# Performance work log

Measured on AMD Instinct MI355X. Metric: run time of the kernel, lower is better.

The kernel has to match this reference:

```python
import jax, jax.numpy as jnp
import numpy as np

B, S, H = 2, 4096, 2048
NH, NKV, D = 16, 4, 128
BS, LOCAL, GLOB, STRIDE = 64, 8, 4, 16
SEL = GLOB + LOCAL
SCALE = D ** -0.5
NEG = -1e9


def rotate_half(x):
    x1, x2 = x[..., : D // 2], x[..., D // 2 :]
    return jnp.concatenate([-x2, x1], axis=-1)


def setup_inputs():
    key = jax.random.key(0)
    ks = jax.random.split(key, 5)
    hidden_states = jax.random.normal(ks[0], (B, S, H), dtype=jnp.float32)
    # standard RoPE tables, shape [B, S, D] as the module expects (cos.unsqueeze(1))
    pos = jnp.arange(S, dtype=jnp.float32)
    inv = 1.0 / (10000.0 ** (jnp.arange(0, D, 2, dtype=jnp.float32) / D))
    freqs = pos[:, None] * inv[None, :]
    emb = jnp.concatenate([freqs, freqs], axis=-1)
    cos = jnp.broadcast_to(jnp.cos(emb)[None], (B, S, D)).astype(jnp.float32)
    sin = jnp.broadcast_to(jnp.sin(emb)[None], (B, S, D)).astype(jnp.float32)
    std = 0.02
    Wq = jax.random.normal(ks[1], (NH * D, H), dtype=jnp.float32) * std
    Wk = jax.random.normal(ks[2], (NKV * D, H), dtype=jnp.float32) * std
    Wv = jax.random.normal(ks[3], (NKV * D, H), dtype=jnp.float32) * std
    Wo = jax.random.normal(ks[4], (H, NH * D), dtype=jnp.float32) * std
    return {"hidden_states": hidden_states, "cos": cos, "sin": sin,
            "Wq": Wq, "Wk": Wk, "Wv": Wv, "Wo": Wo}


def _block_sparse_attn(q, k, v):
    # q, k, v: [B, NH, S, D]; past_len = 0, attention_mask = None (all keys valid)
    qb = S // BS
    kb = S // BS
    qid = jnp.arange(qb)
    # local blocks: the LOCAL most recent blocks ending at the query block
    loc = qid[:, None] - (LOCAL - 1 - jnp.arange(LOCAL)[None, :])
    loc = jnp.clip(loc, 0, kb - 1)
    # global blocks: strided anchors
    g = jnp.clip(jnp.arange(GLOB) * STRIDE, 0, kb - 1)
    glob = jnp.broadcast_to(g[None, :], (qb, GLOB))
    sel = jnp.concatenate([glob, loc], axis=1)  # [qb, SEL]
    valid = sel <= qid[:, None]                 # causal at block level
    # dedup: drop a selected block if an earlier slot selected the same block
    eq = sel[:, :, None] == sel[:, None, :]
    lower = jnp.tril(jnp.ones((SEL, SEL), dtype=bool), k=-1)
    keep = (~(eq & lower[None]).any(-1)) & valid  # [qb, SEL]

    k_blk = k.reshape(B, NH, kb, BS, D)
    v_blk = v.reshape(B, NH, kb, BS, D)
    k_sel = jnp.take(k_blk, sel.reshape(-1), axis=2).reshape(B, NH, qb, SEL * BS, D)
    v_sel = jnp.take(v_blk, sel.reshape(-1), axis=2).reshape(B, NH, qb, SEL * BS, D)
    q_blk = q.reshape(B, NH, qb, BS, D)

    scores = jnp.einsum("bhqid,bhqjd->bhqij", q_blk, k_sel) * SCALE  # [B,NH,qb,BS,SEL*BS]
    keep_tok = jnp.broadcast_to(keep[:, :, None], (qb, SEL, BS)).reshape(qb, SEL * BS)
    scores = scores + (1.0 - keep_tok.astype(scores.dtype))[None, None, :, None, :] * NEG
    # intra-block causal mask where selected block == query block
    same = (sel == qid[:, None]).astype(scores.dtype)  # [qb, SEL]
    intra = jnp.triu(jnp.full((BS, BS), NEG, dtype=scores.dtype), k=1)
    scores6 = scores.reshape(B, NH, qb, BS, SEL, BS)
    scores6 = scores6 + intra[None, None, None, :, None, :] * same[None, None, :, None, :, None]
    scores = scores6.reshape(B, NH, qb, BS, SEL * BS)
    probs = jax.nn.softmax(scores, axis=-1)
    out = jnp.einsum("bhqij,bhqjd->bhqid", probs, v_sel)
    return out.reshape(B, NH, S, D)


def reference(hidden_states, cos, sin, Wq, Wk, Wv, Wo):
    q = (hidden_states @ Wq.T).reshape(B, S, NH, D).transpose(0, 2, 1, 3)
    k = (hidden_states @ Wk.T).reshape(B, S, NKV, D).transpose(0, 2, 1, 3)
    v = (hidden_states @ Wv.T).reshape(B, S, NKV, D).transpose(0, 2, 1, 3)
    c = cos[:, None, :, :]
    s = sin[:, None, :, :]
    q = q * c + rotate_half(q) * s
    k = k * c + rotate_half(k) * s
    rep = NH // NKV
    k = jnp.repeat(k, rep, axis=1)
    v = jnp.repeat(v, rep, axis=1)
    out = _block_sparse_attn(q, k, v)
    out = out.transpose(0, 2, 1, 3).reshape(B, S, NH * D)
    return out @ Wo.T
```

## Files before the change

kernel.cpp:

```cpp
#include <hip/hip_runtime.h>

typedef __bf16 bf16_t;
typedef __bf16 bf16x8_t __attribute__((ext_vector_type(8)));
typedef __bf16 bf16x4_t __attribute__((ext_vector_type(4)));
typedef float f32x4_t __attribute__((ext_vector_type(4)));
typedef unsigned short u16;
typedef unsigned int u32;

#define B_ 2
#define S_ 4096
#define NH_ 16
#define NKV_ 4
#define D_ 128
#define NEG_ (-1000000000.0f)
#define SCALE_ 0.08838834764831845f

__device__ __forceinline__ void load16(const bf16_t* g, bf16_t* l) {
  __builtin_amdgcn_global_load_lds(
      (__attribute__((address_space(1))) void*)(g),
      (__attribute__((address_space(3))) void*)(l),
      16, 0, 0);
}

__global__ __launch_bounds__(256) void cvt_all_kernel(const float* __restrict__ hs,
                                                      const float* __restrict__ Wq,
                                                      const float* __restrict__ Wk,
                                                      const float* __restrict__ Wv,
                                                      const float* __restrict__ Wo,
                                                      bf16_t* __restrict__ Xb,
                                                      bf16_t* __restrict__ Wb,
                                                      bf16_t* __restrict__ Wob) {
  int i = blockIdx.x * 256 + threadIdx.x;
  const float* src; bf16_t* dst; int local;
  if (i < 4194304)      { src = hs; dst = Xb;            local = i; }
  else if (i < 5242880) { src = Wq; dst = Wb;            local = i - 4194304; }
  else if (i < 5505024) { src = Wk; dst = Wb + 4194304;  local = i - 5242880; }
  else if (i < 5767168) { src = Wv; dst = Wb + 5242880;  local = i - 5505024; }
  else                  { src = Wo; dst = Wob;           local = i - 5767168; }
  float4 v = ((const float4*)src)[local];
  bf16x4_t o;
  o.x = (bf16_t)v.x; o.y = (bf16_t)v.y; o.z = (bf16_t)v.z; o.w = (bf16_t)v.w;
  *(bf16x4_t*)(dst + (size_t)local * 4) = o;
}

template <int BF16OUT>
__global__ __launch_bounds__(256) void gemm_bt_kernel(const bf16_t* __restrict__ A,
                                                      const bf16_t* __restrict__ Bm,
                                                      float* __restrict__ Cf,
                                                      bf16_t* __restrict__ Cb,
                                                      int M, int N, int K) {
  __shared__ bf16_t As[128 * 32];
  __shared__ bf16_t Bs[128 * 32];
  const int t = threadIdx.x;
  const int lane = t & 63;
  const int w = t >> 6;
  const int wr = w >> 1, wc = w & 1;
  const int l15 = lane & 15, l4 = lane >> 4;
  const int m0 = blockIdx.x * 128;
  const int n0 = blockIdx.y * 128;
  const int xr = (l15 >> 1) & 3;

  f32x4_t acc[4][4] = {};

  for (int k0 = 0; k0 < K; k0 += 32) {
    __syncthreads();
#pragma unroll
    for (int i = 0; i < 2; i++) {
      int f = t + 256 * i;
      int row = f >> 2, cl = f & 3;
      int cg = cl ^ ((row >> 1) & 3);
      load16(A + (size_t)(m0 + row) * K + k0 + cg * 8, As + (w * 64 + i * 256) * 8);
      load16(Bm + (size_t)(n0 + row) * K + k0 + cg * 8, Bs + (w * 64 + i * 256) * 8);
    }
    __syncthreads();
    bf16x8_t af[4], bfr[4];
#pragma unroll
    for (int mi = 0; mi < 4; mi++) {
      int ra = wr * 64 + mi * 16 + l15;
      af[mi] = *(const bf16x8_t*)&As[(ra * 4 + (l4 ^ xr)) * 8];
    }
#pragma unroll
    for (int ni = 0; ni < 4; ni++) {
      int rb = wc * 64 + ni * 16 + l15;
      bfr[ni] = *(const bf16x8_t*)&Bs[(rb * 4 + (l4 ^ xr)) * 8];
    }
#pragma unroll
    for (int mi = 0; mi < 4; mi++)
#pragma unroll
      for (int ni = 0; ni < 4; ni++)
        acc[mi][ni] = __builtin_amdgcn_mfma_f32_16x16x32_bf16(af[mi], bfr[ni], acc[mi][ni], 0, 0, 0);
  }

#pragma unroll
  for (int mi = 0; mi < 4; mi++)
#pragma unroll
    for (int ni = 0; ni < 4; ni++)
#pragma unroll
      for (int r = 0; r < 4; r++) {
        int grow = m0 + wr * 64 + mi * 16 + l4 * 4 + r;
        int gcol = n0 + wc * 64 + ni * 16 + l15;
        float v = acc[mi][ni][r];
        if (BF16OUT) Cb[(size_t)grow * N + gcol] = (bf16_t)v;
        else Cf[(size_t)grow * N + gcol] = v;
      }
}

__global__ __launch_bounds__(320) void rope_kernel(const bf16_t* __restrict__ qkv,
                                                   const float* __restrict__ cosp,
                                                   const float* __restrict__ sinp,
                                                   bf16_t* __restrict__ Qro,
                                                   bf16_t* __restrict__ Kro) {
  const int tk = blockIdx.x;
  const int b = tk >> 12;
  const int s = tk & 4095;
  const int sblock = s >> 6, row = s & 63;
  const int idx = threadIdx.x;
  int head, lc;
  const bf16_t* base;
  bf16_t* outp;
  if (idx < 256) {
    head = idx >> 4; lc = idx & 15;
    base = qkv + (size_t)tk * 3072 + head * 128;
    outp = Qro + ((size_t)(b * NH_ + head) * 64 + sblock) * 8192;
  } else {
    int i2 = idx - 256;
    head = i2 >> 4; lc = i2 & 15;
    base = qkv + (size_t)tk * 3072 + 2048 + head * 128;
    outp = Kro + ((size_t)(b * NKV_ + head) * 64 + sblock) * 8192;
  }
  const int d0 = lc * 8;
  bf16x8_t x = *(const bf16x8_t*)(base + d0);
  const int d0p = (d0 < 64) ? d0 + 64 : d0 - 64;
  bf16x8_t xp = *(const bf16x8_t*)(base + d0p);
  const float sgn = (d0 < 64) ? -1.0f : 1.0f;
  const float* cb = cosp + (size_t)tk * 128 + d0;
  const float* sb = sinp + (size_t)tk * 128 + d0;
  bf16x8_t o;
#pragma unroll
  for (int e = 0; e < 8; e++)
    o[e] = (bf16_t)((float)x[e] * cb[e] + sgn * (float)xp[e] * sb[e]);
  *(bf16x8_t*)(outp + (lc * 64 + row) * 8) = o;
}

__global__ __launch_bounds__(256) void vtrans_kernel(const u16* __restrict__ qkv,
                                                     u16* __restrict__ vt) {
  __shared__ u16 tile[64][136];
  const int sblock = blockIdx.x;
  const int kh = blockIdx.y;
  const int b = blockIdx.z;
  const int t = threadIdx.x;
#pragma unroll
  for (int i = 0; i < 4; i++) {
    int f = t + 256 * i;
    int sl = f >> 4, c = f & 15;
    uint4 vv = *(const uint4*)(qkv + (size_t)(b * S_ + sblock * 64 + sl) * 3072 + 2560 + kh * 128 + c * 8);
    *(uint4*)&tile[sl][c * 8] = vv;
  }
  __syncthreads();
  u16* out = vt + ((size_t)(b * NKV_ + kh) * 64 + sblock) * 8192;
#pragma unroll
  for (int i = 0; i < 4; i++) {
    int g = t + 256 * i;
    int sc = g >> 7, d = g & 127;
    u16 e0 = tile[sc * 8 + 0][d], e1 = tile[sc * 8 + 1][d];
    u16 e2 = tile[sc * 8 + 2][d], e3 = tile[sc * 8 + 3][d];
    u16 e4 = tile[sc * 8 + 4][d], e5 = tile[sc * 8 + 5][d];
    u16 e6 = tile[sc * 8 + 6][d], e7 = tile[sc * 8 + 7][d];
    uint4 ov;
    ov.x = (u32)e0 | ((u32)e1 << 16);
    ov.y = (u32)e2 | ((u32)e3 << 16);
    ov.z = (u32)e4 | ((u32)e5 << 16);
    ov.w = (u32)e6 | ((u32)e7 << 16);
    *(uint4*)(out + (size_t)g * 8) = ov;
  }
}

__global__ __launch_bounds__(256) void attn_kernel(const bf16_t* __restrict__ Qr,
                                                   const bf16_t* __restrict__ Kr,
                                                   const bf16_t* __restrict__ Vt,
                                                   bf16_t* __restrict__ Ao) {
  __shared__ bf16_t Ks[2][8192];
  __shared__ bf16_t Vs[2][8192];
  __shared__ bf16_t Ps[4 * 16 * 72];
  const int qid = blockIdx.x;
  const int kh = blockIdx.y >> 1;
  const int hp = blockIdx.y & 1;
  const int b = blockIdx.z;
  const int t = threadIdx.x;
  const int lane = t & 63;
  const int w = t >> 6;
  const int l15 = lane & 15, l4 = lane >> 4;
  const int h = kh * 4 + hp * 2 + (w >> 1);
  int row0[2];
  row0[0] = ((w * 2) & 3) * 16;
  row0[1] = ((w * 2 + 1) & 3) * 16;

  int list[12];
  int nkeep = 0;
#pragma unroll
  for (int j = 0; j < 12; j++) {
    int cj;
    if (j < 4) cj = j * 16;
    else { cj = qid - 11 + j; cj = cj < 0 ? 0 : cj; cj = cj > 63 ? 63 : cj; }
    bool keep = (cj <= qid);
#pragma unroll
    for (int i = 0; i < j; i++) {
      int ci;
      if (i < 4) ci = i * 16;
      else { ci = qid - 11 + i; ci = ci < 0 ? 0 : ci; ci = ci > 63 ? 63 : ci; }
      if (ci == cj) keep = false;
    }
    if (keep) list[nkeep++] = cj;
  }

  const bf16_t* Qg = Qr + ((size_t)(b * NH_ + h) * 64 + qid) * 8192;
  const bf16_t* Kg = Kr + ((size_t)(b * NKV_ + kh) * 64) * 8192;
  const bf16_t* Vg = Vt + ((size_t)(b * NKV_ + kh) * 64) * 8192;

  bf16x8_t qa[2][4];
#pragma unroll
  for (int mt = 0; mt < 2; mt++)
#pragma unroll
    for (int ks = 0; ks < 4; ks++)
      qa[mt][ks] = *(const bf16x8_t*)(Qg + ((ks * 4 + l4) * 64 + row0[mt] + l15) * 8);

  bf16x8_t ones;
#pragma unroll
  for (int e = 0; e < 8; e++) ones[e] = (bf16_t)1.0f;

  float mi_r[2][4], li_r[2][4];
  f32x4_t oacc[2][8] = {};
#pragma unroll
  for (int mt = 0; mt < 2; mt++)
#pragma unroll
    for (int r = 0; r < 4; r++) { mi_r[mt][r] = -__builtin_inff(); li_r[mt][r] = 0.0f; }

  {
    int cj = list[0];
#pragma unroll
    for (int i = 0; i < 4; i++) {
      int f = t + 256 * i;
      load16(Kg + (size_t)cj * 8192 + (size_t)f * 8, Ks[0] + (w * 64 + i * 256) * 8);
      load16(Vg + (size_t)cj * 8192 + (size_t)f * 8, Vs[0] + (w * 64 + i * 256) * 8);
    }
  }

  int cur = 0;
#pragma unroll 1
  for (int idx = 0; idx < nkeep; idx++) {
    const int cj = list[idx];
    __syncthreads();
    if (idx + 1 < nkeep) {
      int cn = list[idx + 1];
#pragma unroll
      for (int i = 0; i < 4; i++) {
        int f = t + 256 * i;
        load16(Kg + (size_t)cn * 8192 + (size_t)f * 8, Ks[cur ^ 1] + (w * 64 + i * 256) * 8);
        load16(Vg + (size_t)cn * 8192 + (size_t)f * 8, Vs[cur ^ 1] + (w * 64 + i * 256) * 8);
      }
    }
    const bf16_t* ks_ = Ks[cur];
    const bf16_t* vs_ = Vs[cur];

    f32x4_t sacc[2][4] = {};
#pragma unroll
    for (int ks = 0; ks < 4; ks++)
#pragma unroll
      for (int ni = 0; ni < 4; ni++) {
        bf16x8_t kb = *(const bf16x8_t*)&ks_[((ks * 4 + l4) * 64 + ni * 16 + l15) * 8];
#pragma unroll
        for (int mt = 0; mt < 2; mt++)
          sacc[mt][ni] = __builtin_amdgcn_mfma_f32_16x16x32_bf16(qa[mt][ks], kb, sacc[mt][ni], 0, 0, 0);
      }

    const bool diag = (cj == qid);
    float alpha[2][4];
#pragma unroll
    for (int mt = 0; mt < 2; mt++) {
      float sv[4][4];
#pragma unroll
      for (int ni = 0; ni < 4; ni++)
#pragma unroll
        for (int r = 0; r < 4; r++) {
          float x = sacc[mt][ni][r] * SCALE_;
          if (diag && (ni * 16 + l15) > (row0[mt] + l4 * 4 + r)) x += NEG_;
          sv[ni][r] = x;
        }

      float rmax[4];
#pragma unroll
      for (int r = 0; r < 4; r++)
        rmax[r] = fmaxf(fmaxf(sv[0][r], sv[1][r]), fmaxf(sv[2][r], sv[3][r]));
#pragma unroll
      for (int msk = 1; msk < 16; msk <<= 1)
#pragma unroll
        for (int r = 0; r < 4; r++)
          rmax[r] = fmaxf(rmax[r], __shfl_xor(rmax[r], msk, 64));
#pragma unroll
      for (int r = 0; r < 4; r++) {
        float nm = fmaxf(mi_r[mt][r], rmax[r]);
        alpha[mt][r] = __expf(mi_r[mt][r] - nm);
        mi_r[mt][r] = nm;
      }
      float p[4][4];
#pragma unroll
      for (int ni = 0; ni < 4; ni++)
#pragma unroll
        for (int r = 0; r < 4; r++)
          p[ni][r] = __expf(sv[ni][r] - mi_r[mt][r]);
#pragma unroll
      for (int ni = 0; ni < 4; ni++)
#pragma unroll
        for (int r = 0; r < 4; r++)
          Ps[w * 1152 + (l4 * 4 + r) * 72 + ni * 16 + l15] = (bf16_t)p[ni][r];
#pragma unroll
      for (int n2 = 0; n2 < 8; n2++)
#pragma unroll
        for (int r = 0; r < 4; r++)
          oacc[mt][n2][r] *= alpha[mt][r];

      f32x4_t lacc = {};
#pragma unroll
      for (int kst = 0; kst < 2; kst++) {
        bf16x8_t pa = *(const bf16x8_t*)&Ps[w * 1152 + l15 * 72 + kst * 32 + l4 * 8];
        lacc = __builtin_amdgcn_mfma_f32_16x16x32_bf16(pa, ones, lacc, 0, 0, 0);
#pragma unroll
        for (int n2 = 0; n2 < 8; n2++) {
          bf16x8_t vb = *(const bf16x8_t*)&vs_[((kst * 4 + l4) * 128 + n2 * 16 + l15) * 8];
          oacc[mt][n2] = __builtin_amdgcn_mfma_f32_16x16x32_bf16(pa, vb, oacc[mt][n2], 0, 0, 0);
        }
      }
#pragma unroll
      for (int r = 0; r < 4; r++)
        li_r[mt][r] = li_r[mt][r] * alpha[mt][r] + lacc[r];
    }

    cur ^= 1;
  }

#pragma unroll
  for (int mt = 0; mt < 2; mt++) {
    float invl[4];
#pragma unroll
    for (int r = 0; r < 4; r++) invl[r] = 1.0f / li_r[mt][r];
#pragma unroll
    for (int n2 = 0; n2 < 8; n2++)
#pragma unroll
      for (int r = 0; r < 4; r++) {
        int m = row0[mt] + l4 * 4 + r;
        size_t idx = ((size_t)(b * S_ + qid * 64 + m)) * (NH_ * D_) + h * D_ + n2 * 16 + l15;
        Ao[idx] = (bf16_t)(oacc[mt][n2][r] * invl[r]);
      }
  }
}

extern "C" void kernel_launch(void* const* d_in, const int* in_sizes, int n_in,
                              void* d_out, int out_size, void* d_ws, size_t ws_size,
                              hipStream_t stream) {
  const float* hs = (const float*)d_in[0];
  const float* cosp = (const float*)d_in[1];
  const float* sinp = (const float*)d_in[2];
  const float* Wq = (const float*)d_in[3];
  const float* Wk = (const float*)d_in[4];
  const float* Wv = (const float*)d_in[5];
  const float* Wo = (const float*)d_in[6];
  float* outp = (float*)d_out;

  char* ws = (char*)d_ws;
  bf16_t* Xb   = (bf16_t*)(ws);
  bf16_t* Wb   = (bf16_t*)(ws + 33554432);
  bf16_t* Wob  = (bf16_t*)(ws + 46137344);
  bf16_t* QKVo = (bf16_t*)(ws + 54525952);
  bf16_t* Qr   = (bf16_t*)(ws + 104857600);
  bf16_t* Kr   = (bf16_t*)(ws + 138412032);
  bf16_t* Vt   = (bf16_t*)(ws + 146800640);
  bf16_t* Ao   = QKVo;

  cvt_all_kernel<<<dim3(26624), dim3(256), 0, stream>>>(hs, Wq, Wk, Wv, Wo, Xb, Wb, Wob);

  gemm_bt_kernel<1><<<dim3(64, 24), dim3(256), 0, stream>>>(Xb, Wb, (float*)nullptr, QKVo,
                                                            8192, 3072, 2048);
  rope_kernel<<<dim3(8192), dim3(320), 0, stream>>>(QKVo, cosp, sinp, Qr, Kr);
  vtrans_kernel<<<dim3(64, NKV_, B_), dim3(256), 0, stream>>>((const u16*)QKVo, (u16*)Vt);
  attn_kernel<<<dim3(64, NKV_ * 2, B_), dim3(256), 0, stream>>>(Qr, Kr, Vt, Ao);
  gemm_bt_kernel<0><<<dim3(64, 16), dim3(256), 0, stream>>>(Ao, Wob, outp, (bf16_t*)nullptr,
                                                            8192, 2048, 2048);
}
```

Measured before the change: 531.8 us.

## Triple-buffer GEMM with 256-row tiles, fold softmax scale into Q, lazy rescale

The GEMM is rewritten to use 512-thread blocks with 256x128 tiles and a three-stage global_load_lds pipeline that waits on partial vmcnt with a single barrier per k-step, plus MFMA priority hints. The attention kernel now handles all four heads of a KV group in one 512-thread block, which halves redundant K/V loads. It also pre-scales Q by scale*log2e in the RoPE kernel so softmax can use exp2 without a per-element multiply. Online-softmax rescaling is skipped unless the running max grows by more than a threshold, and the P staging buffer is shrunk. The risks are register pressure and lower occupancy from the larger blocks, and slight numerical drift from the lazy rescale and from scaling Q before bf16 rounding.

Result: faster. 486.3 us (-8.5%).

```diff
diff --git a/kernel.cpp b/kernel.cpp
--- a/kernel.cpp
+++ b/kernel.cpp
@@ -12,8 +12,8 @@
 #define NH_ 16
 #define NKV_ 4
 #define D_ 128
-#define NEG_ (-1000000000.0f)
-#define SCALE_ 0.08838834764831845f
+#define QSCALE_ 0.12751743f
+#define NEG2_ (-1442695040.0f)
 
 __device__ __forceinline__ void load16(const bf16_t* g, bf16_t* l) {
   __builtin_amdgcn_global_load_lds(
@@ -43,53 +43,81 @@
   *(bf16x4_t*)(dst + (size_t)local * 4) = o;
 }
 
+#define DRAIN3() asm volatile("s_waitcnt vmcnt(3)" ::: "memory")
+#define BARF() { __builtin_amdgcn_s_barrier(); asm volatile("" ::: "memory"); }
+
+
+#define PLDA_(PTR) { \
+  _Pragma("unroll") for (int mi = 0; mi < 4; mi++) \
+    a[mi] = *(const bf16x8_t*)&(PTR)[(wr4 * 64 + mi * 16 + l15) * 32 + (l4 ^ xr) * 8]; }
+
+#define PLDB_(PTR) { \
+  _Pragma("unroll") for (int ni = 0; ni < 4; ni++) \
+    b[ni] = *(const bf16x8_t*)&(PTR)[(wc2 * 64 + ni * 16 + l15) * 32 + (l4 ^ xr) * 8]; }
+
+#define PMFMA_() { \
+  __builtin_amdgcn_s_setprio(1); \
+  _Pragma("unroll") for (int mi = 0; mi < 4; mi++) \
+    _Pragma("unroll") for (int ni = 0; ni < 4; ni++) \
+      acc[mi][ni] = __builtin_amdgcn_mfma_f32_16x16x32_bf16(a[mi], b[ni], acc[mi][ni], 0, 0, 0); \
+  __builtin_amdgcn_s_setprio(0); }
+
 template <int BF16OUT>
-__global__ __launch_bounds__(256) void gemm_bt_kernel(const bf16_t* __restrict__ A,
-                                                      const bf16_t* __restrict__ Bm,
-                                                      float* __restrict__ Cf,
-                                                      bf16_t* __restrict__ Cb,
-                                                      int M, int N, int K) {
-  __shared__ bf16_t As[128 * 32];
-  __shared__ bf16_t Bs[128 * 32];
+__global__ __launch_bounds__(512, 2) void gemm_p3_kernel(const bf16_t* __restrict__ A,
+                                                         const bf16_t* __restrict__ Bm,
+                                                         float* __restrict__ Cf,
+                                                         bf16_t* __restrict__ Cb,
+                                                         int M, int N, int K) {
+  __shared__ __align__(16) bf16_t As[3][256][32];
+  __shared__ __align__(16) bf16_t Bs[3][128][32];
   const int t = threadIdx.x;
   const int lane = t & 63;
   const int w = t >> 6;
-  const int wr = w >> 1, wc = w & 1;
+  const int wr4 = w >> 1;
+  const int wc2 = w & 1;
   const int l15 = lane & 15, l4 = lane >> 4;
-  const int m0 = blockIdx.x * 128;
+  const int xr = (l15 >> 1) & 3;
+  const int srow = lane >> 2;
+  const int sg = lane & 3;
+  const int scg = (srow >> 1) & 3;
+
+  const int m0 = blockIdx.x * 256;
   const int n0 = blockIdx.y * 128;
-  const int xr = (l15 >> 1) & 3;
+  const bf16_t* Ablk = A + (size_t)m0 * K;
+  const bf16_t* Bblk = Bm + (size_t)n0 * K;
 
   f32x4_t acc[4][4] = {};
-
-  for (int k0 = 0; k0 < K; k0 += 32) {
-    __syncthreads();
-#pragma unroll
-    for (int i = 0; i < 2; i++) {
-      int f = t + 256 * i;
-      int row = f >> 2, cl = f & 3;
-      int cg = cl ^ ((row >> 1) & 3);
-      load16(A + (size_t)(m0 + row) * K + k0 + cg * 8, As + (w * 64 + i * 256) * 8);
-      load16(Bm + (size_t)(n0 + row) * K + k0 + cg * 8, Bs + (w * 64 + i * 256) * 8);
+  bf16x8_t a[4], b[4];
+
+  const int nkt = K >> 5;
+
+  auto stage = [&](bf16_t* pa, bf16_t* pb, int kt) {
+#pragma unroll
+    for (int c = 0; c < 2; c++) {
+      int r0 = c * 128 + w * 16;
+      load16(Ablk + (size_t)(r0 + srow) * K + kt * 32 + (sg ^ scg) * 8, pa + r0 * 32);
     }
-    __syncthreads();
-    bf16x8_t af[4], bfr[4];
-#pragma unroll
-    for (int mi = 0; mi < 4; mi++) {
-      int ra = wr * 64 + mi * 16 + l15;
-      af[mi] = *(const bf16x8_t*)&As[(ra * 4 + (l4 ^ xr)) * 8];
-    }
-#pragma unroll
-    for (int ni = 0; ni < 4; ni++) {
-      int rb = wc * 64 + ni * 16 + l15;
-      bfr[ni] = *(const bf16x8_t*)&Bs[(rb * 4 + (l4 ^ xr)) * 8];
-    }
-#pragma unroll
-    for (int mi = 0; mi < 4; mi++)
-#pragma unroll
-      for (int ni = 0; ni < 4; ni++)
-        acc[mi][ni] = __builtin_amdgcn_mfma_f32_16x16x32_bf16(af[mi], bfr[ni], acc[mi][ni], 0, 0, 0);
-  }
+    load16(Bblk + (size_t)(w * 16 + srow) * K + kt * 32 + (sg ^ scg) * 8, pb + w * 16 * 32);
+  };
+
+  bf16_t *pa0 = &As[0][0][0], *pa1 = &As[1][0][0], *pa2 = &As[2][0][0];
+  bf16_t *pb0 = &Bs[0][0][0], *pb1 = &Bs[1][0][0], *pb2 = &Bs[2][0][0];
+
+  stage(pa0, pb0, 0);
+  stage(pa1, pb1, 1);
+
+#pragma unroll 1
+  for (int kt = 0; kt < nkt; kt++) {
+    const int ktn = (kt + 2 < nkt) ? kt + 2 : nkt - 1;
+    DRAIN3();
+    BARF();
+    PLDA_(pa0); PLDB_(pb0);
+    stage(pa2, pb2, ktn);
+    PMFMA_();
+    bf16_t* ta = pa0; pa0 = pa1; pa1 = pa2; pa2 = ta;
+    bf16_t* tb = pb0; pb0 = pb1; pb1 = pb2; pb2 = tb;
+  }
+  asm volatile("s_waitcnt vmcnt(0)" ::: "memory");
 
 #pragma unroll
   for (int mi = 0; mi < 4; mi++)
@@ -97,8 +125,8 @@
     for (int ni = 0; ni < 4; ni++)
 #pragma unroll
       for (int r = 0; r < 4; r++) {
-        int grow = m0 + wr * 64 + mi * 16 + l4 * 4 + r;
-        int gcol = n0 + wc * 64 + ni * 16 + l15;
+        int grow = m0 + wr4 * 64 + mi * 16 + l4 * 4 + r;
+        int gcol = n0 + wc2 * 64 + ni * 16 + l15;
         float v = acc[mi][ni][r];
         if (BF16OUT) Cb[(size_t)grow * N + gcol] = (bf16_t)v;
         else Cf[(size_t)grow * N + gcol] = v;
@@ -118,15 +146,18 @@
   int head, lc;
   const bf16_t* base;
   bf16_t* outp;
+  float qs;
   if (idx < 256) {
     head = idx >> 4; lc = idx & 15;
     base = qkv + (size_t)tk * 3072 + head * 128;
     outp = Qro + ((size_t)(b * NH_ + head) * 64 + sblock) * 8192;
+    qs = QSCALE_;
   } else {
     int i2 = idx - 256;
     head = i2 >> 4; lc = i2 & 15;
     base = qkv + (size_t)tk * 3072 + 2048 + head * 128;
     outp = Kro + ((size_t)(b * NKV_ + head) * 64 + sblock) * 8192;
+    qs = 1.0f;
   }
   const int d0 = lc * 8;
   bf16x8_t x = *(const bf16x8_t*)(base + d0);
@@ -138,7 +169,7 @@
   bf16x8_t o;
 #pragma unroll
   for (int e = 0; e < 8; e++)
-    o[e] = (bf16_t)((float)x[e] * cb[e] + sgn * (float)xp[e] * sb[e]);
+    o[e] = (bf16_t)(((float)x[e] * cb[e] + sgn * (float)xp[e] * sb[e]) * qs);
   *(bf16x8_t*)(outp + (lc * 64 + row) * 8) = o;
 }
 
@@ -175,22 +206,21 @@
   }
 }
 
-__global__ __launch_bounds__(256) void attn_kernel(const bf16_t* __restrict__ Qr,
-                                                   const bf16_t* __restrict__ Kr,
-                                                   const bf16_t* __restrict__ Vt,
-                                                   bf16_t* __restrict__ Ao) {
+__global__ __launch_bounds__(512, 2) void attn_kernel(const bf16_t* __restrict__ Qr,
+                                                      const bf16_t* __restrict__ Kr,
+                                                      const bf16_t* __restrict__ Vt,
+                                                      bf16_t* __restrict__ Ao) {
   __shared__ bf16_t Ks[2][8192];
   __shared__ bf16_t Vs[2][8192];
-  __shared__ bf16_t Ps[4 * 16 * 72];
+  __shared__ bf16_t Ps[8 * 640];
   const int qid = blockIdx.x;
-  const int kh = blockIdx.y >> 1;
-  const int hp = blockIdx.y & 1;
+  const int kh = blockIdx.y;
   const int b = blockIdx.z;
   const int t = threadIdx.x;
   const int lane = t & 63;
   const int w = t >> 6;
   const int l15 = lane & 15, l4 = lane >> 4;
-  const int h = kh * 4 + hp * 2 + (w >> 1);
+  const int h = kh * 4 + (w >> 1);
   int row0[2];
   row0[0] = ((w * 2) & 3) * 16;
   row0[1] = ((w * 2 + 1) & 3) * 16;
@@ -238,10 +268,10 @@
   {
     int cj = list[0];
 #pragma unroll
-    for (int i = 0; i < 4; i++) {
-      int f = t + 256 * i;
-      load16(Kg + (size_t)cj * 8192 + (size_t)f * 8, Ks[0] + (w * 64 + i * 256) * 8);
-      load16(Vg + (size_t)cj * 8192 + (size_t)f * 8, Vs[0] + (w * 64 + i * 256) * 8);
+    for (int i = 0; i < 2; i++) {
+      int f = t + 512 * i;
+      load16(Kg + (size_t)cj * 8192 + (size_t)f * 8, Ks[0] + (w * 64 + i * 512) * 8);
+      load16(Vg + (size_t)cj * 8192 + (size_t)f * 8, Vs[0] + (w * 64 + i * 512) * 8);
     }
   }
 
@@ -253,10 +283,10 @@
     if (idx + 1 < nkeep) {
       int cn = list[idx + 1];
 #pragma unroll
-      for (int i = 0; i < 4; i++) {
-        int f = t + 256 * i;
-        load16(Kg + (size_t)cn * 8192 + (size_t)f * 8, Ks[cur ^ 1] + (w * 64 + i * 256) * 8);
-        load16(Vg + (size_t)cn * 8192 + (size_t)f * 8, Vs[cur ^ 1] + (w * 64 + i * 256) * 8);
+      for (int i = 0; i < 2; i++) {
+        int f = t + 512 * i;
+        load16(Kg + (size_t)cn * 8192 + (size_t)f * 8, Ks[cur ^ 1] + (w * 64 + i * 512) * 8);
+        load16(Vg + (size_t)cn * 8192 + (size_t)f * 8, Vs[cur ^ 1] + (w * 64 + i * 512) * 8);
       }
     }
     const bf16_t* ks_ = Ks[cur];
@@ -274,55 +304,61 @@
       }
 
     const bool diag = (cj == qid);
-    float alpha[2][4];
 #pragma unroll
     for (int mt = 0; mt < 2; mt++) {
-      float sv[4][4];
-#pragma unroll
-      for (int ni = 0; ni < 4; ni++)
-#pragma unroll
-        for (int r = 0; r < 4; r++) {
-          float x = sacc[mt][ni][r] * SCALE_;
-          if (diag && (ni * 16 + l15) > (row0[mt] + l4 * 4 + r)) x += NEG_;
-          sv[ni][r] = x;
-        }
-
+      if (diag) {
+#pragma unroll
+        for (int ni = 0; ni < 4; ni++)
+#pragma unroll
+          for (int r = 0; r < 4; r++)
+            if ((ni * 16 + l15) > (row0[mt] + l4 * 4 + r)) sacc[mt][ni][r] += NEG2_;
+      }
       float rmax[4];
 #pragma unroll
       for (int r = 0; r < 4; r++)
-        rmax[r] = fmaxf(fmaxf(sv[0][r], sv[1][r]), fmaxf(sv[2][r], sv[3][r]));
+        rmax[r] = fmaxf(fmaxf(sacc[mt][0][r], sacc[mt][1][r]),
+                        fmaxf(sacc[mt][2][r], sacc[mt][3][r]));
 #pragma unroll
       for (int msk = 1; msk < 16; msk <<= 1)
 #pragma unroll
         for (int r = 0; r < 4; r++)
           rmax[r] = fmaxf(rmax[r], __shfl_xor(rmax[r], msk, 64));
-#pragma unroll
-      for (int r = 0; r < 4; r++) {
-        float nm = fmaxf(mi_r[mt][r], rmax[r]);
-        alpha[mt][r] = __expf(mi_r[mt][r] - nm);
-        mi_r[mt][r] = nm;
+      bool need = false;
+#pragma unroll
+      for (int r = 0; r < 4; r++) need = need || (rmax[r] > mi_r[mt][r] + 8.0f);
+      if (__any(need)) {
+        float alpha[4];
+#pragma unroll
+        for (int r = 0; r < 4; r++) {
+          float nm = fmaxf(mi_r[mt][r], rmax[r]);
+          alpha[r] = exp2f(mi_r[mt][r] - nm);
+          mi_r[mt][r] = nm;
+        }
+#pragma unroll
+        for (int n2 = 0; n2 < 8; n2++)
+#pragma unroll
+          for (int r = 0; r < 4; r++)
+            oacc[mt][n2][r] *= alpha[r];
+#pragma unroll
+        for (int r = 0; r < 4; r++) li_r[mt][r] *= alpha[r];
       }
       float p[4][4];
 #pragma unroll
       for (int ni = 0; ni < 4; ni++)
 #pragma unroll
         for (int r = 0; r < 4; r++)
-          p[ni][r] = __expf(sv[ni][r] - mi_r[mt][r]);
-#pragma unroll
-      for (int ni = 0; ni < 4; ni++)
-#pragma unroll
-        for (int r = 0; r < 4; r++)
-          Ps[w * 1152 + (l4 * 4 + r) * 72 + ni * 16 + l15] = (bf16_t)p[ni][r];
-#pragma unroll
-      for (int n2 = 0; n2 < 8; n2++)
-#pragma unroll
-        for (int r = 0; r < 4; r++)
-          oacc[mt][n2][r] *= alpha[mt][r];
-
+          p[ni][r] = exp2f(sacc[mt][ni][r] - mi_r[mt][r]);
+
+      bf16_t* psw = &Ps[w * 640];
       f32x4_t lacc = {};
 #pragma unroll
       for (int kst = 0; kst < 2; kst++) {
-        bf16x8_t pa = *(const bf16x8_t*)&Ps[w * 1152 + l15 * 72 + kst * 32 + l4 * 8];
+#pragma unroll
+        for (int n2i = 0; n2i < 2; n2i++)
+#pragma unroll
+          for (int r = 0; r < 4; r++)
+            psw[(l4 * 4 + r) * 40 + n2i * 16 + l15] = (bf16_t)p[kst * 2 + n2i][r];
+        bf16x8_t pa = *(const bf16x8_t*)&psw[l15 * 40 + l4 * 8];
         lacc = __builtin_amdgcn_mfma_f32_16x16x32_bf16(pa, ones, lacc, 0, 0, 0);
 #pragma unroll
         for (int n2 = 0; n2 < 8; n2++) {
@@ -332,7 +368,7 @@
       }
 #pragma unroll
       for (int r = 0; r < 4; r++)
-        li_r[mt][r] = li_r[mt][r] * alpha[mt][r] + lacc[r];
+        li_r[mt][r] += lacc[r];
     }
 
     cur ^= 1;
@@ -378,11 +414,11 @@
 
   cvt_all_kernel<<<dim3(26624), dim3(256), 0, stream>>>(hs, Wq, Wk, Wv, Wo, Xb, Wb, Wob);
 
-  gemm_bt_kernel<1><<<dim3(64, 24), dim3(256), 0, stream>>>(Xb, Wb, (float*)nullptr, QKVo,
+  gemm_p3_kernel<1><<<dim3(32, 24), dim3(512), 0, stream>>>(Xb, Wb, (float*)nullptr, QKVo,
                                                             8192, 3072, 2048);
   rope_kernel<<<dim3(8192), dim3(320), 0, stream>>>(QKVo, cosp, sinp, Qr, Kr);
   vtrans_kernel<<<dim3(64, NKV_, B_), dim3(256), 0, stream>>>((const u16*)QKVo, (u16*)Vt);
-  attn_kernel<<<dim3(64, NKV_ * 2, B_), dim3(256), 0, stream>>>(Qr, Kr, Vt, Ao);
-  gemm_bt_kernel<0><<<dim3(64, 16), dim3(256), 0, stream>>>(Ao, Wob, outp, (bf16_t*)nullptr,
+  attn_kernel<<<dim3(64, NKV_, B_), dim3(512), 0, stream>>>(Qr, Kr, Vt, Ao);
+  gemm_p3_kernel<0><<<dim3(32, 16), dim3(512), 0, stream>>>(Ao, Wob, outp, (bf16_t*)nullptr,
                                                             8192, 2048, 2048);
 }
```
